# Performance work log

Hardware: AMD Instinct MI355X
Metric: run time of the kernel (lower is better)

Reference implementation:

```python
import jax, jax.numpy as jnp
import numpy as np

N_NODES = 100000
N_EDGES = 600000
N_GRAPHS = 256
K = 5
N_FEAT = 16
N_CLASSES = 4


def setup_inputs() -> dict:
    key = jax.random.key(0)
    ks = jax.random.split(key, 12)
    x = jax.random.normal(ks[0], (N_NODES, N_FEAT), dtype=jnp.float32)
    edge_index = jax.random.randint(ks[1], (2, N_EDGES), 0, N_NODES, dtype=jnp.int32)
    batch = jnp.sort(jax.random.randint(ks[2], (N_NODES,), 0, N_GRAPHS, dtype=jnp.int32))
    s = 0.1
    W11 = jax.random.normal(ks[3], (K, N_FEAT, 64), dtype=jnp.float32) * s
    b11 = jnp.zeros((64,), dtype=jnp.float32)
    W12 = jax.random.normal(ks[4], (K, N_FEAT, 64), dtype=jnp.float32) * s
    b12 = jnp.zeros((64,), dtype=jnp.float32)
    W21 = jax.random.normal(ks[5], (K, 128, 256), dtype=jnp.float32) * s
    b21 = jnp.zeros((256,), dtype=jnp.float32)
    W22 = jax.random.normal(ks[6], (K, 128, 256), dtype=jnp.float32) * s
    b22 = jnp.zeros((256,), dtype=jnp.float32)
    fc_w = jax.random.normal(ks[7], (512, N_CLASSES), dtype=jnp.float32) * s
    fc_b = jnp.zeros((N_CLASSES,), dtype=jnp.float32)
    return {
        "x": x, "edge_index": edge_index, "batch": batch,
        "W11": W11, "b11": b11, "W12": W12, "b12": b12,
        "W21": W21, "b21": b21, "W22": W22, "b22": b22,
        "fc_w": fc_w, "fc_b": fc_b,
    }


def _cheb_norm(src, dst, n_nodes):
    # PyG ChebConv (sym norm, lambda_max=2): L_hat = -D^{-1/2} A D^{-1/2},
    # zero diagonal. Degree computed over source (row) indices.
    deg = jax.ops.segment_sum(jnp.ones_like(src, dtype=jnp.float32), src,
                              num_segments=n_nodes)
    dinv = jnp.where(deg > 0, jax.lax.rsqrt(jnp.maximum(deg, 1.0)), 0.0)
    return -dinv[src] * dinv[dst]


def _cheb_conv(x, src, dst, w_norm, W, b):
    # Chebyshev recursion: Tx0=x, Tx1=L_hat x, Txk = 2 L_hat Tx_{k-1} - Tx_{k-2}
    n = x.shape[0]

    def spmm(h):  # aggregate messages from src at dst
        return jax.ops.segment_sum(h[src] * w_norm[:, None], dst, num_segments=n)

    Tx0 = x
    Tx1 = spmm(x)
    out = jnp.einsum('nf,fo->no', Tx0, W[0]) + jnp.einsum('nf,fo->no', Tx1, W[1])
    for k in range(2, W.shape[0]):
        Tx2 = 2.0 * spmm(Tx1) - Tx0
        out = out + jnp.einsum('nf,fo->no', Tx2, W[k])
        Tx0, Tx1 = Tx1, Tx2
    return out + b


def reference(x, edge_index, batch, W11, b11, W12, b12, W21, b21, W22, b22,
              fc_w, fc_b):
    src, dst = edge_index[0], edge_index[1]
    w_fwd = _cheb_norm(src, dst, N_NODES)
    w_rev = _cheb_norm(dst, src, N_NODES)  # reversed adjacency

    x1 = jax.nn.relu(_cheb_conv(x, src, dst, w_fwd, W11, b11))
    x2 = jax.nn.relu(_cheb_conv(x, dst, src, w_rev, W12, b12))
    h = jnp.concatenate([x1, x2], axis=1)  # [N, 128]

    x1 = jax.nn.relu(_cheb_conv(h, src, dst, w_fwd, W21, b21))
    x2 = jax.nn.relu(_cheb_conv(h, dst, src, w_rev, W22, b22))
    h = jnp.concatenate([x1, x2], axis=1)  # [N, 512]

    # global mean pool over graphs
    sums = jax.ops.segment_sum(h, batch, num_segments=N_GRAPHS)
    cnt = jax.ops.segment_sum(jnp.ones((h.shape[0],), dtype=h.dtype), batch,
                              num_segments=N_GRAPHS)
    pooled = sums / jnp.maximum(cnt, 1.0)[:, None]  # [G, 512]

    logits = pooled @ fc_w + fc_b
    return jax.nn.log_softmax(logits, axis=1)
```

## Files before the change

### kernel.cpp

```cpp
#include <hip/hip_runtime.h>
#include <stdint.h>

#define NNODES 100000
#define NEDGES 600000
#define NGRAPH 256
#define KCH 5
#define F1 16
#define O1 64
#define F2 128
#define O2 256
#define FT1 (KCH * F1)
#define FT2 (KCH * F2)
#define KSTEPS 20
#define KS1 3
#define NBK 10
#define LROW2 72
#define NXCD 8

typedef unsigned short ushort_t;
typedef __attribute__((ext_vector_type(8))) short bf16x8;
typedef __attribute__((ext_vector_type(4))) float f32x4;

__device__ __forceinline__ float bflo(unsigned int u) {
    union { unsigned int u; float f; } v; v.u = u << 16; return v.f;
}
__device__ __forceinline__ float bfhi(unsigned int u) {
    union { unsigned int u; float f; } v; v.u = u & 0xFFFF0000u; return v.f;
}
__device__ __forceinline__ unsigned int f2bf(float f) {
    union { float f; unsigned int u; } v; v.f = f;
    return (v.u + 0x7FFFu + ((v.u >> 16) & 1u)) >> 16;
}
__device__ __forceinline__ unsigned int pack2(float lo, float hi) {
    return (f2bf(hi) << 16) | f2bf(lo);
}


__global__ void k_count(const int* __restrict__ src, const int* __restrict__ dst,
                        int* __restrict__ cntDst, int* __restrict__ cntSrc, int E) {
    int e = blockIdx.x * 256 + threadIdx.x;
    if (e < E) {
        atomicAdd(&cntDst[dst[e]], 1);
        atomicAdd(&cntSrc[src[e]], 1);
    }
}

__global__ void k_dinv(const int* __restrict__ cntDst, const int* __restrict__ cntSrc,
                       float* __restrict__ dinvF, float* __restrict__ dinvR, int n) {
    int i = blockIdx.x * 256 + threadIdx.x;
    if (i < n) {
        int cs = cntSrc[i], cd = cntDst[i];
        dinvF[i] = cs > 0 ? rsqrtf((float)cs) : 0.f;
        dinvR[i] = cd > 0 ? rsqrtf((float)cd) : 0.f;
    }
}

__global__ void k_scan1(const int* __restrict__ in, int* __restrict__ out,
                        int* __restrict__ blksum, int n) {
    __shared__ int a[512];
    __shared__ int s[256];
    int t = threadIdx.x;
    int base = blockIdx.x * 512;
    a[t]       = (base + t < n)       ? in[base + t]       : 0;
    a[t + 256] = (base + t + 256 < n) ? in[base + t + 256] : 0;
    __syncthreads();
    s[t] = a[2 * t] + a[2 * t + 1];
    __syncthreads();
    for (int off = 1; off < 256; off <<= 1) {
        int v = (t >= off) ? s[t - off] : 0;
        __syncthreads();
        s[t] += v;
        __syncthreads();
    }
    int ep = (t > 0) ? s[t - 1] : 0;
    if (base + 2 * t < n)     out[base + 2 * t]     = ep;
    if (base + 2 * t + 1 < n) out[base + 2 * t + 1] = ep + a[2 * t];
    if (t == 255) blksum[blockIdx.x] = s[255];
}

__global__ void k_scan2(int* __restrict__ blksum, int nb) {
    __shared__ int s[256];
    int t = threadIdx.x;
    s[t] = (t < nb) ? blksum[t] : 0;
    __syncthreads();
    for (int off = 1; off < 256; off <<= 1) {
        int v = (t >= off) ? s[t - off] : 0;
        __syncthreads();
        s[t] += v;
        __syncthreads();
    }
    if (t < nb) blksum[t] = (t > 0) ? s[t - 1] : 0;
}

__global__ void k_scan3(int* __restrict__ out, const int* __restrict__ blksum, int n) {
    int i = blockIdx.x * 512 + threadIdx.x;
    int add = blksum[blockIdx.x];
    if (i < n) out[i] += add;
    if (i + 256 < n) out[i + 256] += add;
}

__global__ void k_tail(int* __restrict__ off_f, int* __restrict__ off_r, int n, int E) {
    if (threadIdx.x == 0) { off_f[n] = E; off_r[n] = E; }
}

__global__ void k_scatter(const int* __restrict__ src, const int* __restrict__ dst,
                          const float* __restrict__ dinvF, const float* __restrict__ dinvR,
                          int* __restrict__ curF, int* __restrict__ curR,
                          int2* __restrict__ edF, int2* __restrict__ edR, int E,
                          int chunk) {
    int c = blockIdx.x & (NXCD - 1);
    int sb = blockIdx.x >> 3;
    int slices = gridDim.x >> 3;
    int lo = c * chunk, hi = lo + chunk;
    for (int e = sb * 256 + threadIdx.x; e < E; e += slices * 256) {
        int s = src[e], d = dst[e];
        if (d >= lo && d < hi) {
            int p = atomicAdd(&curF[d], 1);
            float wf = -dinvF[s] * dinvF[d];
            edF[p] = make_int2(s, __float_as_int(wf));
        }
        if (s >= lo && s < hi) {
            int q = atomicAdd(&curR[s], 1);
            float wr = -dinvR[s] * dinvR[d];
            edR[q] = make_int2(d, __float_as_int(wr));
        }
    }
}

__global__ void k_gstart(const int* __restrict__ batch, int* __restrict__ gstart, int n) {
    int g = blockIdx.x * 64 + threadIdx.x;
    if (g > NGRAPH) return;
    if (g == NGRAPH) { gstart[g] = n; return; }
    int lo = 0, hi = n;
    while (lo < hi) {
        int mid = (lo + hi) >> 1;
        if (batch[mid] < g) lo = mid + 1; else hi = mid;
    }
    gstart[g] = lo;
}


__global__ void k_copyx(const float* __restrict__ x, float* __restrict__ Tx, int n) {
    int tid = blockIdx.x * 256 + threadIdx.x;
    int r = tid >> 2, c = tid & 3;
    if (r < n)
        *(float4*)(Tx + (size_t)r * FT1 + c * 4) =
            *(const float4*)(x + (size_t)r * 16 + c * 4);
}

__global__ void k_spmm_f32(const float* __restrict__ Hin, float* __restrict__ Hout,
                           const float* __restrict__ Tx0,
                           const int* __restrict__ off, const int2* __restrict__ ed,
                           int n) {
    int tid = blockIdx.x * 256 + threadIdx.x;
    int r = tid >> 2, c = tid & 3;
    if (r >= n) return;
    int j0 = off[r], j1 = off[r + 1];
    float4 s = {0.f, 0.f, 0.f, 0.f};
    int j = j0;
    for (; j + 4 <= j1; j += 4) {
        int2 e0 = ed[j], e1 = ed[j + 1], e2 = ed[j + 2], e3 = ed[j + 3];
        float wa = __int_as_float(e0.y), wb = __int_as_float(e1.y);
        float wc = __int_as_float(e2.y), wd = __int_as_float(e3.y);
        const float4 h0 = *(const float4*)(Hin + (size_t)e0.x * FT1 + c * 4);
        const float4 h1 = *(const float4*)(Hin + (size_t)e1.x * FT1 + c * 4);
        const float4 h2 = *(const float4*)(Hin + (size_t)e2.x * FT1 + c * 4);
        const float4 h3 = *(const float4*)(Hin + (size_t)e3.x * FT1 + c * 4);
        s.x += wa * h0.x; s.y += wa * h0.y; s.z += wa * h0.z; s.w += wa * h0.w;
        s.x += wb * h1.x; s.y += wb * h1.y; s.z += wb * h1.z; s.w += wb * h1.w;
        s.x += wc * h2.x; s.y += wc * h2.y; s.z += wc * h2.z; s.w += wc * h2.w;
        s.x += wd * h3.x; s.y += wd * h3.y; s.z += wd * h3.z; s.w += wd * h3.w;
    }
    for (; j < j1; ++j) {
        int2 e = ed[j];
        float w2 = __int_as_float(e.y);
        const float4 h = *(const float4*)(Hin + (size_t)e.x * FT1 + c * 4);
        s.x += w2 * h.x; s.y += w2 * h.y; s.z += w2 * h.z; s.w += w2 * h.w;
    }
    float4 o;
    if (Tx0) {
        const float4 t0 = *(const float4*)(Tx0 + (size_t)r * FT1 + c * 4);
        o.x = 2.f * s.x - t0.x; o.y = 2.f * s.y - t0.y;
        o.z = 2.f * s.z - t0.z; o.w = 2.f * s.w - t0.w;
    } else {
        o = s;
    }
    *(float4*)(Hout + (size_t)r * FT1 + c * 4) = o;
}

__global__ void k_spmm_bf(const ushort_t* __restrict__ Hin, ushort_t* __restrict__ Hout,
                          const ushort_t* __restrict__ Tx0,
                          const int* __restrict__ off, const int2* __restrict__ ed,
                          int n) {
    int r = blockIdx.x * 4 + (threadIdx.x >> 6);
    r = __builtin_amdgcn_readfirstlane(r);
    int c = threadIdx.x & 63;
    if (r >= n) return;
    int j0 = __builtin_amdgcn_readfirstlane(off[r]);
    int j1 = __builtin_amdgcn_readfirstlane(off[r + 1]);
    float s0 = 0.f, s1 = 0.f;
    int j = j0;
    int jfull = j0 + ((j1 - j0) & ~7);
    for (; j < jfull; j += 8) {
        float w[8];
        unsigned int h[8];
#pragma unroll
        for (int sl = 0; sl < 8; ++sl) {
            int2 e = ed[j + sl];
            w[sl] = __int_as_float(e.y);
            h[sl] = *(const unsigned int*)(Hin + (size_t)e.x * FT2 + c * 2);
        }
#pragma unroll
        for (int sl = 0; sl < 8; ++sl) {
            s0 = fmaf(bflo(h[sl]), w[sl], s0);
            s1 = fmaf(bfhi(h[sl]), w[sl], s1);
        }
    }
    int rem = j1 - j;
    if (rem) {
        float w[8];
        unsigned int h[8];
#pragma unroll
        for (int sl = 0; sl < 8; ++sl) {
            w[sl] = 0.f; h[sl] = 0u;
            if (sl < rem) {
                int2 e = ed[j + sl];
                w[sl] = __int_as_float(e.y);
                h[sl] = *(const unsigned int*)(Hin + (size_t)e.x * FT2 + c * 2);
            }
        }
#pragma unroll
        for (int sl = 0; sl < 8; ++sl) {
            s0 = fmaf(bflo(h[sl]), w[sl], s0);
            s1 = fmaf(bfhi(h[sl]), w[sl], s1);
        }
    }
    if (Tx0) {
        unsigned int t0 = *(const unsigned int*)(Tx0 + (size_t)r * FT2 + c * 2);
        s0 = 2.f * s0 - bflo(t0);
        s1 = 2.f * s1 - bfhi(t0);
    }
    *(unsigned int*)(Hout + (size_t)r * FT2 + c * 2) = pack2(s0, s1);
}

__global__ void k_packW1(const float* __restrict__ W, ushort_t* __restrict__ Bp) {
    int tid = blockIdx.x * 256 + threadIdx.x;
    if (tid >= 4 * KS1 * 64) return;
    int lane = tid & 63;
    int ks = (tid >> 6) % KS1;
    int nt = tid / (64 * KS1);
    int k0 = ks * 32 + (lane >> 4) * 8;
    int ncol = nt * 16 + (lane & 15);
    float v[8];
#pragma unroll
    for (int j = 0; j < 8; ++j) {
        int k = k0 + j;
        v[j] = (k < FT1) ? W[(size_t)k * O1 + ncol] : 0.f;
    }
    uint4 o;
    o.x = pack2(v[0], v[1]); o.y = pack2(v[2], v[3]);
    o.z = pack2(v[4], v[5]); o.w = pack2(v[6], v[7]);
    *(uint4*)(Bp + (size_t)tid * 8) = o;
}

__global__ __launch_bounds__(256) void k_gemm1_mfma(
    const float* __restrict__ A, const ushort_t* __restrict__ Bp,
    const float* __restrict__ bias, ushort_t* __restrict__ out, int n) {
    int lane = threadIdx.x & 63;
    int wvi = threadIdx.x >> 6;
    int mrow = lane & 15;
    int quad = lane >> 4;
    int m0w = blockIdx.x * 64 + wvi * 16;
    int row = m0w + mrow;
    int rowc = row < n ? row : n - 1;
    const float* Ar = A + (size_t)rowc * FT1 + quad * 8;

    f32x4 acc[4] = {};
#pragma unroll
    for (int ks = 0; ks < KS1; ++ks) {
        float4 a0 = *(const float4*)(Ar + ks * 32);
        float4 a1 = *(const float4*)(Ar + ks * 32 + 4);
        union { bf16x8 v; unsigned int u[4]; } ua;
        ua.u[0] = pack2(a0.x, a0.y);
        ua.u[1] = pack2(a0.z, a0.w);
        ua.u[2] = pack2(a1.x, a1.y);
        ua.u[3] = pack2(a1.z, a1.w);
#pragma unroll
        for (int nf = 0; nf < 4; ++nf) {
            bf16x8 bfr = *(const bf16x8*)(Bp + ((size_t)(nf * KS1 + ks) * 64 + lane) * 8);
            acc[nf] = __builtin_amdgcn_mfma_f32_16x16x32_bf16(ua.v, bfr, acc[nf], 0, 0, 0);
        }
    }
#pragma unroll
    for (int nf = 0; nf < 4; ++nf) {
        float bb = bias[nf * 16 + mrow];
#pragma unroll
        for (int reg = 0; reg < 4; ++reg) {
            int orow = m0w + quad * 4 + reg;
            if (orow < n)
                out[(size_t)orow * FT2 + nf * 16 + mrow] =
                    (ushort_t)f2bf(fmaxf(acc[nf][reg] + bb, 0.f));
        }
    }
}

__global__ void k_packW(const float* __restrict__ W, ushort_t* __restrict__ Bp) {
    int tid = blockIdx.x * 256 + threadIdx.x;
    if (tid >= 16 * KSTEPS * 64) return;
    int lane = tid & 63;
    int ks = (tid >> 6) % KSTEPS;
    int nt = tid / (64 * KSTEPS);
    int k0 = ks * 32 + (lane >> 4) * 8;
    int ncol = nt * 16 + (lane & 15);
    float v[8];
#pragma unroll
    for (int j = 0; j < 8; ++j) v[j] = W[(size_t)(k0 + j) * O2 + ncol];
    uint4 o;
    o.x = pack2(v[0], v[1]); o.y = pack2(v[2], v[3]);
    o.z = pack2(v[4], v[5]); o.w = pack2(v[6], v[7]);
    *(uint4*)(Bp + (size_t)tid * 8) = o;
}

__global__ __launch_bounds__(256) void k_gemm2_mfma(
    const ushort_t* __restrict__ A, const ushort_t* __restrict__ Bp,
    const float* __restrict__ bias, float* __restrict__ pooled, int colofs,
    const int* __restrict__ batch, int n) {
    __shared__ ushort_t lds[2][64 * LROW2];

    int lane = threadIdx.x & 63;
    int wv = threadIdx.x >> 6;
    int m0 = blockIdx.x * 64;
    int mrow = lane & 15;
    int quad = lane >> 4;
    int srow = threadIdx.x >> 2;
    int sc = threadIdx.x & 3;

    const ushort_t* Ag = A + (size_t)(m0 + srow) * FT2 + sc * 8;
    const ushort_t* Bbase = Bp + ((size_t)(wv * 4) * KSTEPS * 64 + lane) * 8;
    int sidx = srow * LROW2 + sc * 8;

    f32x4 acc[4][4] = {};
    uint4 nxt0, nxt1;
    bf16x8 bcur[4], bnxt[4];

    *(uint4*)&lds[0][sidx]      = *(const uint4*)(Ag);
    *(uint4*)&lds[0][sidx + 32] = *(const uint4*)(Ag + 32);
    nxt0 = *(const uint4*)(Ag + 64);
    nxt1 = *(const uint4*)(Ag + 96);
#pragma unroll
    for (int nf = 0; nf < 4; ++nf)
        bcur[nf] = *(const bf16x8*)(Bbase + ((size_t)nf * KSTEPS) * 512);

    for (int bk = 0; bk < NBK; ++bk) {
        __syncthreads();
        if (bk + 1 < NBK) {
            *(uint4*)&lds[(bk + 1) & 1][sidx]      = nxt0;
            *(uint4*)&lds[(bk + 1) & 1][sidx + 32] = nxt1;
        }
        if (bk + 2 < NBK) {
            nxt0 = *(const uint4*)(Ag + (bk + 2) * 64);
            nxt1 = *(const uint4*)(Ag + (bk + 2) * 64 + 32);
        }
        const ushort_t* lbuf = &lds[bk & 1][0];
#pragma unroll
        for (int sub = 0; sub < 2; ++sub) {
            int ks = bk * 2 + sub;
            if (ks + 1 < KSTEPS) {
#pragma unroll
                for (int nf = 0; nf < 4; ++nf)
                    bnxt[nf] = *(const bf16x8*)(Bbase + ((size_t)nf * KSTEPS + ks + 1) * 512);
            }
            bf16x8 af[4];
#pragma unroll
            for (int mf = 0; mf < 4; ++mf)
                af[mf] = *(const bf16x8*)(lbuf + (mf * 16 + mrow) * LROW2 + sub * 32 + quad * 8);
#pragma unroll
            for (int mf = 0; mf < 4; ++mf)
#pragma unroll
                for (int nf = 0; nf < 4; ++nf)
                    acc[mf][nf] = __builtin_amdgcn_mfma_f32_16x16x32_bf16(
                        af[mf], bcur[nf], acc[mf][nf], 0, 0, 0);
#pragma unroll
            for (int nf = 0; nf < 4; ++nf) bcur[nf] = bnxt[nf];
        }
    }

    float bcol[4];
#pragma unroll
    for (int nf = 0; nf < 4; ++nf) bcol[nf] = bias[wv * 64 + nf * 16 + mrow];

#pragma unroll
    for (int mf = 0; mf < 4; ++mf) {
        int t0 = m0 + mf * 16;
        if (t0 >= n) break;
        int te = (t0 + 15 < n) ? t0 + 15 : n - 1;
        int r0 = t0 + quad * 4;
        if (batch[t0] == batch[te]) {
            int g = batch[t0];
#pragma unroll
            for (int nf = 0; nf < 4; ++nf) {
                float s = 0.f;
#pragma unroll
                for (int reg = 0; reg < 4; ++reg) {
                    float v = fmaxf(acc[mf][nf][reg] + bcol[nf], 0.f);
                    if (r0 + reg < n) s += v;
                }
                s += __shfl_xor(s, 16, 64);
                s += __shfl_xor(s, 32, 64);
                if (quad == 0)
                    atomicAdd(pooled + (size_t)g * 512 + colofs + wv * 64 + nf * 16 + mrow, s);
            }
        } else {
            int gb[4];
#pragma unroll
            for (int reg = 0; reg < 4; ++reg)
                gb[reg] = batch[(r0 + reg < n) ? r0 + reg : n - 1];
#pragma unroll
            for (int nf = 0; nf < 4; ++nf) {
                int col = colofs + wv * 64 + nf * 16 + mrow;
                float run = 0.f;
                int g = gb[0];
                bool any = false;
#pragma unroll
                for (int reg = 0; reg < 4; ++reg) {
                    int row = r0 + reg;
                    if (row >= n) break;
                    float v = fmaxf(acc[mf][nf][reg] + bcol[nf], 0.f);
                    if (gb[reg] != g) {
                        atomicAdd(pooled + (size_t)g * 512 + col, run);
                        run = 0.f;
                        g = gb[reg];
                    }
                    run += v;
                    any = true;
                }
                if (any) atomicAdd(pooled + (size_t)g * 512 + col, run);
            }
        }
    }
}

__global__ void k_logits(const float* __restrict__ pooled, const int* __restrict__ gstart,
                         const float* __restrict__ fcw, const float* __restrict__ fcb,
                         float* __restrict__ out) {
    int g = threadIdx.x;
    int cnt = gstart[g + 1] - gstart[g];
    float inv = 1.f / (float)(cnt > 1 ? cnt : 1);
    float lg[4];
#pragma unroll
    for (int o = 0; o < 4; ++o) lg[o] = fcb[o];
    for (int f = 0; f < 512; ++f) {
        float p = pooled[g * 512 + f] * inv;
#pragma unroll
        for (int o = 0; o < 4; ++o) lg[o] = fmaf(p, fcw[f * 4 + o], lg[o]);
    }
    float m = fmaxf(fmaxf(lg[0], lg[1]), fmaxf(lg[2], lg[3]));
    float s = 0.f;
#pragma unroll
    for (int o = 0; o < 4; ++o) s += expf(lg[o] - m);
    float l = logf(s);
#pragma unroll
    for (int o = 0; o < 4; ++o) out[g * 4 + o] = lg[o] - m - l;
}


extern "C" void kernel_launch(void* const* d_in, const int* in_sizes, int n_in,
                              void* d_out, int out_size, void* d_ws, size_t ws_size,
                              hipStream_t stream) {
    const float* x   = (const float*)d_in[0];
    const int* ei    = (const int*)d_in[1];
    const int* batch = (const int*)d_in[2];
    const float* W11 = (const float*)d_in[3];
    const float* b11 = (const float*)d_in[4];
    const float* W12 = (const float*)d_in[5];
    const float* b12 = (const float*)d_in[6];
    const float* W21 = (const float*)d_in[7];
    const float* b21 = (const float*)d_in[8];
    const float* W22 = (const float*)d_in[9];
    const float* b22 = (const float*)d_in[10];
    const float* fcw = (const float*)d_in[11];
    const float* fcb = (const float*)d_in[12];
    float* out = (float*)d_out;

    const int N = in_sizes[0] / F1;
    const int E = in_sizes[1] / 2;
    const int* src = ei;
    const int* dst = ei + E;

    char* w = (char*)d_ws;
    size_t pos = 0;
    auto alloc = [&](size_t bytes) -> void* {
        void* p = w + pos;
        pos += (bytes + 255) & ~(size_t)255;
        return p;
    };
    int* cur_f   = (int*)alloc((size_t)N * 4);
    int* cur_r   = (int*)alloc((size_t)N * 4);
    int* off_f   = (int*)alloc((size_t)(N + 1) * 4);
    int* off_r   = (int*)alloc((size_t)(N + 1) * 4);
    float* dinvF = (float*)alloc((size_t)N * 4);
    float* dinvR = (float*)alloc((size_t)N * 4);
    int2* ed_f   = (int2*)alloc((size_t)E * 8);
    int2* ed_r   = (int2*)alloc((size_t)E * 8);
    int* blks_f  = (int*)alloc(1024);
    int* blks_r  = (int*)alloc(1024);
    int* gstart  = (int*)alloc((NGRAPH + 1) * 4);
    float* pooled = (float*)alloc((size_t)NGRAPH * 512 * 4);
    ushort_t* BpF = (ushort_t*)alloc((size_t)FT2 * O2 * 2);
    ushort_t* BpR = (ushort_t*)alloc((size_t)FT2 * O2 * 2);
    ushort_t* Bp1F = (ushort_t*)alloc((size_t)4 * KS1 * 64 * 8 * 2);
    ushort_t* Bp1R = (ushort_t*)alloc((size_t)4 * KS1 * 64 * 8 * 2);
    float* TxAll1 = (float*)alloc(((size_t)N * FT1 + 256) * 4);
    ushort_t* TxAll2 = (ushort_t*)alloc((size_t)(N + 64) * FT2 * 2);

    (void)hipMemsetAsync(cur_f, 0, (size_t)N * 4, stream);
    (void)hipMemsetAsync(cur_r, 0, (size_t)N * 4, stream);
    (void)hipMemsetAsync(pooled, 0, (size_t)NGRAPH * 512 * 4, stream);

    int gE = (E + 255) / 256, gN = (N + 255) / 256;
    k_count<<<gE, 256, 0, stream>>>(src, dst, cur_f, cur_r, E);
    k_dinv<<<gN, 256, 0, stream>>>(cur_f, cur_r, dinvF, dinvR, N);

    int NB = (N + 511) / 512;
    k_scan1<<<NB, 256, 0, stream>>>(cur_f, off_f, blks_f, N);
    k_scan1<<<NB, 256, 0, stream>>>(cur_r, off_r, blks_r, N);
    k_scan2<<<1, 256, 0, stream>>>(blks_f, NB);
    k_scan2<<<1, 256, 0, stream>>>(blks_r, NB);
    k_scan3<<<NB, 256, 0, stream>>>(off_f, blks_f, N);
    k_scan3<<<NB, 256, 0, stream>>>(off_r, blks_r, N);
    k_tail<<<1, 64, 0, stream>>>(off_f, off_r, N, E);
    (void)hipMemcpyAsync(cur_f, off_f, (size_t)N * 4, hipMemcpyDeviceToDevice, stream);
    (void)hipMemcpyAsync(cur_r, off_r, (size_t)N * 4, hipMemcpyDeviceToDevice, stream);
    int chunk = (N + NXCD - 1) / NXCD;
    k_scatter<<<NXCD * 256, 256, 0, stream>>>(src, dst, dinvF, dinvR, cur_f, cur_r,
                                              ed_f, ed_r, E, chunk);
    k_gstart<<<5, 64, 0, stream>>>(batch, gstart, N);
    k_packW<<<80, 256, 0, stream>>>(W21, BpF);
    k_packW<<<80, 256, 0, stream>>>(W22, BpR);
    k_packW1<<<3, 256, 0, stream>>>(W11, Bp1F);
    k_packW1<<<3, 256, 0, stream>>>(W12, Bp1R);

    k_copyx<<<(N * 4 + 255) / 256, 256, 0, stream>>>(x, TxAll1, N);
    int gs1 = (N * 4 + 255) / 256;
    int gg1 = (N + 63) / 64;
    auto C1 = [&](int k) { return TxAll1 + k * F1; };
    k_spmm_f32<<<gs1, 256, 0, stream>>>(C1(0), C1(1), nullptr, off_f, ed_f, N);
    k_spmm_f32<<<gs1, 256, 0, stream>>>(C1(1), C1(2), C1(0), off_f, ed_f, N);
    k_spmm_f32<<<gs1, 256, 0, stream>>>(C1(2), C1(3), C1(1), off_f, ed_f, N);
    k_spmm_f32<<<gs1, 256, 0, stream>>>(C1(3), C1(4), C1(2), off_f, ed_f, N);
    k_gemm1_mfma<<<gg1, 256, 0, stream>>>(TxAll1, Bp1F, b11, TxAll2, N);
    k_spmm_f32<<<gs1, 256, 0, stream>>>(C1(0), C1(1), nullptr, off_r, ed_r, N);
    k_spmm_f32<<<gs1, 256, 0, stream>>>(C1(1), C1(2), C1(0), off_r, ed_r, N);
    k_spmm_f32<<<gs1, 256, 0, stream>>>(C1(2), C1(3), C1(1), off_r, ed_r, N);
    k_spmm_f32<<<gs1, 256, 0, stream>>>(C1(3), C1(4), C1(2), off_r, ed_r, N);
    k_gemm1_mfma<<<gg1, 256, 0, stream>>>(TxAll1, Bp1R, b12, TxAll2 + O1, N);

    int gs2 = (N + 3) / 4;
    auto C2 = [&](int k) { return TxAll2 + k * F2; };
    int gg = (N + 63) / 64;
    k_spmm_bf<<<gs2, 256, 0, stream>>>(C2(0), C2(1), nullptr, off_f, ed_f, N);
    k_spmm_bf<<<gs2, 256, 0, stream>>>(C2(1), C2(2), C2(0), off_f, ed_f, N);
    k_spmm_bf<<<gs2, 256, 0, stream>>>(C2(2), C2(3), C2(1), off_f, ed_f, N);
    k_spmm_bf<<<gs2, 256, 0, stream>>>(C2(3), C2(4), C2(2), off_f, ed_f, N);
    k_gemm2_mfma<<<gg, 256, 0, stream>>>(TxAll2, BpF, b21, pooled, 0, batch, N);
    k_spmm_bf<<<gs2, 256, 0, stream>>>(C2(0), C2(1), nullptr, off_r, ed_r, N);
    k_spmm_bf<<<gs2, 256, 0, stream>>>(C2(1), C2(2), C2(0), off_r, ed_r, N);
    k_spmm_bf<<<gs2, 256, 0, stream>>>(C2(2), C2(3), C2(1), off_r, ed_r, N);
    k_spmm_bf<<<gs2, 256, 0, stream>>>(C2(3), C2(4), C2(2), off_r, ed_r, N);
    k_gemm2_mfma<<<gg, 256, 0, stream>>>(TxAll2, BpR, b22, pooled, 256, batch, N);

    k_logits<<<1, 256, 0, stream>>>(pooled, gstart, fcw, fcb, out);
}
```

Measured before the change: 788.8 us.

## Gather bf16 copies in layer-1 SpMM, widen gemm2 tile, fuse cursor copy

Layer-1 SpMM now gathers neighbour features from a compact bf16 shadow buffer, written alongside the fp32 output, instead of strided fp32 rows. This halves gather bytes and improves cache density, at the cost of bf16 rounding in the recursion inputs. The gemm2 MFMA kernel now uses 512 threads and 128-row tiles so each B fragment load is shared by two M halves. The scan finalize also writes the cursor arrays directly, removing two device-to-device memcpys.

Measured after the change: 794.2 us. No clear change (+0.7%).

```diff
diff --git a/kernel.cpp b/kernel.cpp
--- a/kernel.cpp
+++ b/kernel.cpp
@@ -92,11 +92,12 @@
     if (t < nb) blksum[t] = (t > 0) ? s[t - 1] : 0;
 }
 
-__global__ void k_scan3(int* __restrict__ out, const int* __restrict__ blksum, int n) {
+__global__ void k_scan3(int* __restrict__ out, int* __restrict__ cur,
+                        const int* __restrict__ blksum, int n) {
     int i = blockIdx.x * 512 + threadIdx.x;
     int add = blksum[blockIdx.x];
-    if (i < n) out[i] += add;
-    if (i + 256 < n) out[i + 256] += add;
+    if (i < n)       { int v = out[i] + add;       out[i] = v;       cur[i] = v; }
+    if (i + 256 < n) { int v = out[i + 256] + add; out[i + 256] = v; cur[i + 256] = v; }
 }
 
 __global__ void k_tail(int* __restrict__ off_f, int* __restrict__ off_r, int n, int E) {
@@ -140,15 +141,22 @@
 }
 
 
-__global__ void k_copyx(const float* __restrict__ x, float* __restrict__ Tx, int n) {
+__global__ void k_copyx(const float* __restrict__ x, float* __restrict__ Tx,
+                        ushort_t* __restrict__ TxB, int n) {
     int tid = blockIdx.x * 256 + threadIdx.x;
     int r = tid >> 2, c = tid & 3;
-    if (r < n)
-        *(float4*)(Tx + (size_t)r * FT1 + c * 4) =
-            *(const float4*)(x + (size_t)r * 16 + c * 4);
-}
-
-__global__ void k_spmm_f32(const float* __restrict__ Hin, float* __restrict__ Hout,
+    if (r < n) {
+        float4 v = *(const float4*)(x + (size_t)r * 16 + c * 4);
+        *(float4*)(Tx + (size_t)r * FT1 + c * 4) = v;
+        uint2 b;
+        b.x = pack2(v.x, v.y);
+        b.y = pack2(v.z, v.w);
+        *(uint2*)(TxB + (size_t)r * F1 + c * 4) = b;
+    }
+}
+
+__global__ void k_spmm_f32(const ushort_t* __restrict__ HinB, float* __restrict__ Hout,
+                           ushort_t* __restrict__ HoutB,
                            const float* __restrict__ Tx0,
                            const int* __restrict__ off, const int2* __restrict__ ed,
                            int n) {
@@ -162,20 +170,25 @@
         int2 e0 = ed[j], e1 = ed[j + 1], e2 = ed[j + 2], e3 = ed[j + 3];
         float wa = __int_as_float(e0.y), wb = __int_as_float(e1.y);
         float wc = __int_as_float(e2.y), wd = __int_as_float(e3.y);
-        const float4 h0 = *(const float4*)(Hin + (size_t)e0.x * FT1 + c * 4);
-        const float4 h1 = *(const float4*)(Hin + (size_t)e1.x * FT1 + c * 4);
-        const float4 h2 = *(const float4*)(Hin + (size_t)e2.x * FT1 + c * 4);
-        const float4 h3 = *(const float4*)(Hin + (size_t)e3.x * FT1 + c * 4);
-        s.x += wa * h0.x; s.y += wa * h0.y; s.z += wa * h0.z; s.w += wa * h0.w;
-        s.x += wb * h1.x; s.y += wb * h1.y; s.z += wb * h1.z; s.w += wb * h1.w;
-        s.x += wc * h2.x; s.y += wc * h2.y; s.z += wc * h2.z; s.w += wc * h2.w;
-        s.x += wd * h3.x; s.y += wd * h3.y; s.z += wd * h3.z; s.w += wd * h3.w;
+        const uint2 h0 = *(const uint2*)(HinB + (size_t)e0.x * F1 + c * 4);
+        const uint2 h1 = *(const uint2*)(HinB + (size_t)e1.x * F1 + c * 4);
+        const uint2 h2 = *(const uint2*)(HinB + (size_t)e2.x * F1 + c * 4);
+        const uint2 h3 = *(const uint2*)(HinB + (size_t)e3.x * F1 + c * 4);
+        s.x = fmaf(wa, bflo(h0.x), s.x); s.y = fmaf(wa, bfhi(h0.x), s.y);
+        s.z = fmaf(wa, bflo(h0.y), s.z); s.w = fmaf(wa, bfhi(h0.y), s.w);
+        s.x = fmaf(wb, bflo(h1.x), s.x); s.y = fmaf(wb, bfhi(h1.x), s.y);
+        s.z = fmaf(wb, bflo(h1.y), s.z); s.w = fmaf(wb, bfhi(h1.y), s.w);
+        s.x = fmaf(wc, bflo(h2.x), s.x); s.y = fmaf(wc, bfhi(h2.x), s.y);
+        s.z = fmaf(wc, bflo(h2.y), s.z); s.w = fmaf(wc, bfhi(h2.y), s.w);
+        s.x = fmaf(wd, bflo(h3.x), s.x); s.y = fmaf(wd, bfhi(h3.x), s.y);
+        s.z = fmaf(wd, bflo(h3.y), s.z); s.w = fmaf(wd, bfhi(h3.y), s.w);
     }
     for (; j < j1; ++j) {
         int2 e = ed[j];
         float w2 = __int_as_float(e.y);
-        const float4 h = *(const float4*)(Hin + (size_t)e.x * FT1 + c * 4);
-        s.x += w2 * h.x; s.y += w2 * h.y; s.z += w2 * h.z; s.w += w2 * h.w;
+        const uint2 h = *(const uint2*)(HinB + (size_t)e.x * F1 + c * 4);
+        s.x = fmaf(w2, bflo(h.x), s.x); s.y = fmaf(w2, bfhi(h.x), s.y);
+        s.z = fmaf(w2, bflo(h.y), s.z); s.w = fmaf(w2, bfhi(h.y), s.w);
     }
     float4 o;
     if (Tx0) {
@@ -186,6 +199,10 @@
         o = s;
     }
     *(float4*)(Hout + (size_t)r * FT1 + c * 4) = o;
+    uint2 b;
+    b.x = pack2(o.x, o.y);
+    b.y = pack2(o.z, o.w);
+    *(uint2*)(HoutB + (size_t)r * F1 + c * 4) = b;
 }
 
 __global__ void k_spmm_bf(const ushort_t* __restrict__ Hin, ushort_t* __restrict__ Hout,
@@ -321,23 +338,26 @@
     *(uint4*)(Bp + (size_t)tid * 8) = o;
 }
 
-__global__ __launch_bounds__(256) void k_gemm2_mfma(
+__global__ __launch_bounds__(512) void k_gemm2_mfma(
     const ushort_t* __restrict__ A, const ushort_t* __restrict__ Bp,
     const float* __restrict__ bias, float* __restrict__ pooled, int colofs,
     const int* __restrict__ batch, int n) {
-    __shared__ ushort_t lds[2][64 * LROW2];
+    __shared__ ushort_t lds[2][128 * LROW2];
 
     int lane = threadIdx.x & 63;
     int wv = threadIdx.x >> 6;
-    int m0 = blockIdx.x * 64;
+    int mhalf = wv >> 2;
+    int nquad = wv & 3;
+    int m0 = blockIdx.x * 128;
     int mrow = lane & 15;
     int quad = lane >> 4;
     int srow = threadIdx.x >> 2;
     int sc = threadIdx.x & 3;
 
     const ushort_t* Ag = A + (size_t)(m0 + srow) * FT2 + sc * 8;
-    const ushort_t* Bbase = Bp + ((size_t)(wv * 4) * KSTEPS * 64 + lane) * 8;
+    const ushort_t* Bbase = Bp + ((size_t)(nquad * 4) * KSTEPS * 64 + lane) * 8;
     int sidx = srow * LROW2 + sc * 8;
+    int rbase = (mhalf * 64) * LROW2;
 
     f32x4 acc[4][4] = {};
     uint4 nxt0, nxt1;
@@ -373,7 +393,8 @@
             bf16x8 af[4];
 #pragma unroll
             for (int mf = 0; mf < 4; ++mf)
-                af[mf] = *(const bf16x8*)(lbuf + (mf * 16 + mrow) * LROW2 + sub * 32 + quad * 8);
+                af[mf] = *(const bf16x8*)(lbuf + rbase + (mf * 16 + mrow) * LROW2 +
+                                          sub * 32 + quad * 8);
 #pragma unroll
             for (int mf = 0; mf < 4; ++mf)
 #pragma unroll
@@ -387,11 +408,11 @@
 
     float bcol[4];
 #pragma unroll
-    for (int nf = 0; nf < 4; ++nf) bcol[nf] = bias[wv * 64 + nf * 16 + mrow];
+    for (int nf = 0; nf < 4; ++nf) bcol[nf] = bias[nquad * 64 + nf * 16 + mrow];
 
 #pragma unroll
     for (int mf = 0; mf < 4; ++mf) {
-        int t0 = m0 + mf * 16;
+        int t0 = m0 + mhalf * 64 + mf * 16;
         if (t0 >= n) break;
         int te = (t0 + 15 < n) ? t0 + 15 : n - 1;
         int r0 = t0 + quad * 4;
@@ -408,7 +429,7 @@
                 s += __shfl_xor(s, 16, 64);
                 s += __shfl_xor(s, 32, 64);
                 if (quad == 0)
-                    atomicAdd(pooled + (size_t)g * 512 + colofs + wv * 64 + nf * 16 + mrow, s);
+                    atomicAdd(pooled + (size_t)g * 512 + colofs + nquad * 64 + nf * 16 + mrow, s);
             }
         } else {
             int gb[4];
@@ -417,7 +438,7 @@
                 gb[reg] = batch[(r0 + reg < n) ? r0 + reg : n - 1];
 #pragma unroll
             for (int nf = 0; nf < 4; ++nf) {
-                int col = colofs + wv * 64 + nf * 16 + mrow;
+                int col = colofs + nquad * 64 + nf * 16 + mrow;
                 float run = 0.f;
                 int g = gb[0];
                 bool any = false;
@@ -511,7 +532,8 @@
     ushort_t* Bp1F = (ushort_t*)alloc((size_t)4 * KS1 * 64 * 8 * 2);
     ushort_t* Bp1R = (ushort_t*)alloc((size_t)4 * KS1 * 64 * 8 * 2);
     float* TxAll1 = (float*)alloc(((size_t)N * FT1 + 256) * 4);
-    ushort_t* TxAll2 = (ushort_t*)alloc((size_t)(N + 64) * FT2 * 2);
+    ushort_t* TxB1 = (ushort_t*)alloc((size_t)KCH * N * F1 * 2);
+    ushort_t* TxAll2 = (ushort_t*)alloc((size_t)(N + 128) * FT2 * 2);
 
     (void)hipMemsetAsync(cur_f, 0, (size_t)N * 4, stream);
     (void)hipMemsetAsync(cur_r, 0, (size_t)N * 4, stream);
@@ -526,11 +548,9 @@
     k_scan1<<<NB, 256, 0, stream>>>(cur_r, off_r, blks_r, N);
     k_scan2<<<1, 256, 0, stream>>>(blks_f, NB);
     k_scan2<<<1, 256, 0, stream>>>(blks_r, NB);
-    k_scan3<<<NB, 256, 0, stream>>>(off_f, blks_f, N);
-    k_scan3<<<NB, 256, 0, stream>>>(off_r, blks_r, N);
+    k_scan3<<<NB, 256, 0, stream>>>(off_f, cur_f, blks_f, N);
+    k_scan3<<<NB, 256, 0, stream>>>(off_r, cur_r, blks_r, N);
     k_tail<<<1, 64, 0, stream>>>(off_f, off_r, N, E);
-    (void)hipMemcpyAsync(cur_f, off_f, (size_t)N * 4, hipMemcpyDeviceToDevice, stream);
-    (void)hipMemcpyAsync(cur_r, off_r, (size_t)N * 4, hipMemcpyDeviceToDevice, stream);
     int chunk = (N + NXCD - 1) / NXCD;
     k_scatter<<<NXCD * 256, 256, 0, stream>>>(src, dst, dinvF, dinvR, cur_f, cur_r,
                                               ed_f, ed_r, E, chunk);
@@ -540,34 +560,35 @@
     k_packW1<<<3, 256, 0, stream>>>(W11, Bp1F);
     k_packW1<<<3, 256, 0, stream>>>(W12, Bp1R);
 
-    k_copyx<<<(N * 4 + 255) / 256, 256, 0, stream>>>(x, TxAll1, N);
+    k_copyx<<<(N * 4 + 255) / 256, 256, 0, stream>>>(x, TxAll1, TxB1, N);
     int gs1 = (N * 4 + 255) / 256;
     int gg1 = (N + 63) / 64;
     auto C1 = [&](int k) { return TxAll1 + k * F1; };
-    k_spmm_f32<<<gs1, 256, 0, stream>>>(C1(0), C1(1), nullptr, off_f, ed_f, N);
-    k_spmm_f32<<<gs1, 256, 0, stream>>>(C1(1), C1(2), C1(0), off_f, ed_f, N);
-    k_spmm_f32<<<gs1, 256, 0, stream>>>(C1(2), C1(3), C1(1), off_f, ed_f, N);
-    k_spmm_f32<<<gs1, 256, 0, stream>>>(C1(3), C1(4), C1(2), off_f, ed_f, N);
+    auto B1 = [&](int k) { return TxB1 + (size_t)k * N * F1; };
+    k_spmm_f32<<<gs1, 256, 0, stream>>>(B1(0), C1(1), B1(1), nullptr, off_f, ed_f, N);
+    k_spmm_f32<<<gs1, 256, 0, stream>>>(B1(1), C1(2), B1(2), C1(0), off_f, ed_f, N);
+    k_spmm_f32<<<gs1, 256, 0, stream>>>(B1(2), C1(3), B1(3), C1(1), off_f, ed_f, N);
+    k_spmm_f32<<<gs1, 256, 0, stream>>>(B1(3), C1(4), B1(4), C1(2), off_f, ed_f, N);
     k_gemm1_mfma<<<gg1, 256, 0, stream>>>(TxAll1, Bp1F, b11, TxAll2, N);
-    k_spmm_f32<<<gs1, 256, 0, stream>>>(C1(0), C1(1), nullptr, off_r, ed_r, N);
-    k_spmm_f32<<<gs1, 256, 0, stream>>>(C1(1), C1(2), C1(0), off_r, ed_r, N);
-    k_spmm_f32<<<gs1, 256, 0, stream>>>(C1(2), C1(3), C1(1), off_r, ed_r, N);
-    k_spmm_f32<<<gs1, 256, 0, stream>>>(C1(3), C1(4), C1(2), off_r, ed_r, N);
+    k_spmm_f32<<<gs1, 256, 0, stream>>>(B1(0), C1(1), B1(1), nullptr, off_r, ed_r, N);
+    k_spmm_f32<<<gs1, 256, 0, stream>>>(B1(1), C1(2), B1(2), C1(0), off_r, ed_r, N);
+    k_spmm_f32<<<gs1, 256, 0, stream>>>(B1(2), C1(3), B1(3), C1(1), off_r, ed_r, N);
+    k_spmm_f32<<<gs1, 256, 0, stream>>>(B1(3), C1(4), B1(4), C1(2), off_r, ed_r, N);
     k_gemm1_mfma<<<gg1, 256, 0, stream>>>(TxAll1, Bp1R, b12, TxAll2 + O1, N);
 
     int gs2 = (N + 3) / 4;
     auto C2 = [&](int k) { return TxAll2 + k * F2; };
-    int gg = (N + 63) / 64;
+    int gg = (N + 127) / 128;
     k_spmm_bf<<<gs2, 256, 0, stream>>>(C2(0), C2(1), nullptr, off_f, ed_f, N);
     k_spmm_bf<<<gs2, 256, 0, stream>>>(C2(1), C2(2), C2(0), off_f, ed_f, N);
     k_spmm_bf<<<gs2, 256, 0, stream>>>(C2(2), C2(3), C2(1), off_f, ed_f, N);
     k_spmm_bf<<<gs2, 256, 0, stream>>>(C2(3), C2(4), C2(2), off_f, ed_f, N);
-    k_gemm2_mfma<<<gg, 256, 0, stream>>>(TxAll2, BpF, b21, pooled, 0, batch, N);
+    k_gemm2_mfma<<<gg, 512, 0, stream>>>(TxAll2, BpF, b21, pooled, 0, batch, N);
     k_spmm_bf<<<gs2, 256, 0, stream>>>(C2(0), C2(1), nullptr, off_r, ed_r, N);
     k_spmm_bf<<<gs2, 256, 0, stream>>>(C2(1), C2(2), C2(0), off_r, ed_r, N);
     k_spmm_bf<<<gs2, 256, 0, stream>>>(C2(2), C2(3), C2(1), off_r, ed_r, N);
     k_spmm_bf<<<gs2, 256, 0, stream>>>(C2(3), C2(4), C2(2), off_r, ed_r, N);
-    k_gemm2_mfma<<<gg, 256, 0, stream>>>(TxAll2, BpR, b22, pooled, 256, batch, N);
+    k_gemm2_mfma<<<gg, 512, 0, stream>>>(TxAll2, BpR, b22, pooled, 256, batch, N);
 
     k_logits<<<1, 256, 0, stream>>>(pooled, gstart, fcw, fcb, out);
 }
```
